# Performance work log

Measured on AMD Instinct MI355X. Metric: run time of the kernel, lower is better.

Reference implementation:

```python
import jax, jax.numpy as jnp
import numpy as np

N_NODES = 100000
N_EDGES = 1600000
N_GRAPHS = 256
IN_F = 64   # global_features (GNN input dim)
OUT_F = 64  # node_features (GNN output dim)


def setup_inputs() -> dict:
    key = jax.random.key(0)
    ks = jax.random.split(key, 8)
    x = jax.random.normal(ks[0], (N_NODES, IN_F), dtype=jnp.float32)
    edge_index = jax.random.randint(ks[1], (2, N_EDGES), 0, N_NODES, dtype=jnp.int64)
    batch = jnp.sort(jax.random.randint(ks[2], (N_NODES,), 0, N_GRAPHS, dtype=jnp.int64))
    # GNNLayer linear: in=global_features, out=node_features
    W_gnn = jax.random.normal(ks[3], (IN_F, OUT_F), dtype=jnp.float32) / np.sqrt(IN_F)
    b_gnn = jnp.zeros((OUT_F,), dtype=jnp.float32)
    # global_attention: Linear(node_features, 1)
    W_att = jax.random.normal(ks[4], (OUT_F, 1), dtype=jnp.float32) / np.sqrt(OUT_F)
    b_att = jnp.zeros((1,), dtype=jnp.float32)
    return {"x": x, "edge_index": edge_index, "batch": batch,
            "W_gnn": W_gnn, "b_gnn": b_gnn, "W_att": W_att, "b_att": b_att}


def reference(x, edge_index, batch, W_gnn, b_gnn, W_att, b_att):
    src, dst = edge_index[0], edge_index[1]
    # --- GNN message passing layer: aggregate neighbor features, transform ---
    agg = jax.ops.segment_sum(x[src], dst, num_segments=N_NODES)  # [N, IN_F]
    h = jax.nn.relu((x + agg) @ W_gnn + b_gnn)                    # [N, OUT_F]
    # --- attention scores + scatter softmax over batch segments ---
    scores = (h @ W_att + b_att)[:, 0]                            # [N]
    seg_max = jax.ops.segment_max(scores, batch, num_segments=N_GRAPHS)
    e = jnp.exp(scores - seg_max[batch])
    denom = jax.ops.segment_sum(e, batch, num_segments=N_GRAPHS)
    w = e / denom[batch]                                          # [N]
    # --- weighted scatter-add pooling ---
    out = jax.ops.segment_sum(w[:, None] * h, batch, num_segments=N_GRAPHS)
    return out  # [N_GRAPHS, OUT_F]
```

## Files before the change

### kernel.cpp

```cpp
#include <hip/hip_runtime.h>

#define N_NODES  100000
#define N_EDGES  1600000
#define N_GRAPHS 256
#define F        64

#define CHUNK    8192
#define NCHUNK   196
#define GBN      128
#define NB2      782
#define EDGE_CAP 2560

__device__ __forceinline__ unsigned short f2bf(float f) {
    unsigned int u = __float_as_uint(f);
    u += 0x7FFFu + ((u >> 16) & 1u);
    return (unsigned short)(u >> 16);
}
__global__ __launch_bounds__(256) void cast_kernel(
        const float* __restrict__ x, unsigned short* __restrict__ xh) {
    int i = blockIdx.x * 256 + threadIdx.x;
    float4 v = ((const float4*)x)[i];
    ushort4 o;
    o.x = f2bf(v.x); o.y = f2bf(v.y); o.z = f2bf(v.z); o.w = f2bf(v.w);
    ((ushort4*)xh)[i] = o;
}

__global__ __launch_bounds__(1024) void scatter_sort_kernel(
        const int* __restrict__ src, const int* __restrict__ dst,
        unsigned int* __restrict__ pairs, int* __restrict__ cstartT) {
    __shared__ int hist[NB2];
    __shared__ int cur[NB2];
    __shared__ int scan[1024];
    __shared__ unsigned int stage[CHUNK];
    int tid  = threadIdx.x;
    int c    = blockIdx.x;
    int base = c * CHUNK;
    int m    = min(CHUNK, N_EDGES - base);

    for (int b = tid; b < NB2; b += 1024) hist[b] = 0;
    __syncthreads();
    for (int e = tid; e < m; e += 1024)
        atomicAdd(&hist[dst[base + e] >> 7], 1);
    __syncthreads();
    scan[tid] = (tid < NB2) ? hist[tid] : 0;
    __syncthreads();
    #pragma unroll
    for (int o = 1; o < 1024; o <<= 1) {
        int u = (tid >= o) ? scan[tid - o] : 0;
        __syncthreads();
        scan[tid] += u;
        __syncthreads();
    }
    if (tid < NB2) {
        int excl = scan[tid] - hist[tid];
        cur[tid] = excl;
        cstartT[tid * NCHUNK + c] = base + excl;
    }
    if (tid == 0) cstartT[NB2 * NCHUNK + c] = base + m;
    __syncthreads();
    for (int e = tid; e < m; e += 1024) {
        int d = dst[base + e];
        int slot = atomicAdd(&cur[d >> 7], 1);
        stage[slot] = ((unsigned)(d & (GBN - 1)) << 17) | (unsigned)src[base + e];
    }
    __syncthreads();
    for (int e = tid; e < m; e += 1024)
        pairs[base + e] = stage[e];
}

__device__ __forceinline__ float bfl(unsigned int u) { return __uint_as_float(u << 16); }
__device__ __forceinline__ float bfh(unsigned int u) { return __uint_as_float(u & 0xFFFF0000u); }

__global__ __launch_bounds__(512) void gather_pool_kernel(
        const unsigned short* __restrict__ xh,
        const unsigned int*   __restrict__ pairs,
        const int*   __restrict__ cstartT,
        const int*   __restrict__ batch,
        const float* __restrict__ Wg,
        const float* __restrict__ bg,
        const float* __restrict__ Wa,
        const float* __restrict__ ba,
        float*       __restrict__ out_acc,
        float*       __restrict__ denom) {
    __shared__ int rstart[NCHUNK];
    __shared__ int rcnt[NCHUNK];
    __shared__ int roff[NCHUNK];
    __shared__ int sc[256];
    __shared__ int Etot_s;
    __shared__ unsigned int epairs[EDGE_CAP];
    __shared__ unsigned int esrc[EDGE_CAP];
    __shared__ int ncnt[GBN];
    __shared__ int nstart[GBN];
    __shared__ int ncur[GBN];

    int tid   = threadIdx.x;
    int wave  = tid >> 6;
    int lane  = tid & 63;
    int b     = blockIdx.x;
    int node0 = b * GBN;
    int nn    = min(GBN, N_NODES - node0);

    if (tid < NCHUNK) {
        int a = cstartT[b * NCHUNK + tid];
        int n = cstartT[(b + 1) * NCHUNK + tid];
        rstart[tid] = a;
        rcnt[tid]   = n - a;
    }
    __syncthreads();
    if (tid < 256) sc[tid] = (tid < NCHUNK) ? rcnt[tid] : 0;
    __syncthreads();
    #pragma unroll
    for (int o = 1; o < 256; o <<= 1) {
        int u = (tid < 256 && tid >= o) ? sc[tid - o] : 0;
        __syncthreads();
        if (tid < 256) sc[tid] += u;
        __syncthreads();
    }
    if (tid < NCHUNK) roff[tid] = sc[tid] - rcnt[tid];
    if (tid == 0) Etot_s = sc[NCHUNK - 1];
    __syncthreads();
    int E = Etot_s;

    for (int r = wave; r < NCHUNK; r += 8) {
        int cr = rcnt[r];
        for (int l = lane; l < cr; l += 64)
            epairs[roff[r] + l] = pairs[rstart[r] + l];
    }
    __syncthreads();

    if (tid < GBN) ncnt[tid] = 0;
    __syncthreads();
    for (int e = tid; e < E; e += 512)
        atomicAdd(&ncnt[epairs[e] >> 17], 1);
    __syncthreads();
    if (tid < 128) sc[tid] = ncnt[tid];
    __syncthreads();
    #pragma unroll
    for (int o = 1; o < 128; o <<= 1) {
        int u = (tid < 128 && tid >= o) ? sc[tid - o] : 0;
        __syncthreads();
        if (tid < 128) sc[tid] += u;
        __syncthreads();
    }
    if (tid < GBN) {
        int excl = sc[tid] - ncnt[tid];
        nstart[tid] = excl;
        ncur[tid]   = excl;
    }
    __syncthreads();
    for (int e = tid; e < E; e += 512) {
        unsigned int p = epairs[e];
        int slot = atomicAdd(&ncur[p >> 17], 1);
        esrc[slot] = p & 0x1FFFFu;
    }
    __syncthreads();

    int grp = lane >> 3;
    int cc  = lane & 7;

    float wcol[F];
    #pragma unroll
    for (int k = 0; k < F; ++k) wcol[k] = Wg[k * F + lane];
    float bgl = bg[lane];
    float wal = Wa[lane];
    float ba0 = ba[0];

    const uint4* xh4 = (const uint4*)xh;

    int r0 = wave * 16;
    if (r0 < nn) {
        int rEnd = min(r0 + 16, nn);
        int   cur_g = batch[node0 + r0];
        float accw  = 0.f;
        float denw  = 0.f;

        for (int r = r0; r < rEnd; ++r) {
            int n     = node0 + r;
            int start = nstart[r];
            int end   = start + ncnt[r];

            float a0=0.f,a1=0.f,a2=0.f,a3=0.f,a4=0.f,a5=0.f,a6=0.f,a7=0.f;
            for (int bs = start; bs < end; bs += 64) {
                int jmax = end - bs; if (jmax > 64) jmax = 64;
                int sl = (bs + lane < end) ? (int)esrc[bs + lane] : 0;
                for (int j = 0; j < jmax; j += 8) {
                    int el = j + grp;
                    int s  = __shfl(sl, el, 64);
                    if (el < jmax) {
                        uint4 v = xh4[s * 8 + cc];
                        a0 += bfl(v.x); a1 += bfh(v.x);
                        a2 += bfl(v.y); a3 += bfh(v.y);
                        a4 += bfl(v.z); a5 += bfh(v.z);
                        a6 += bfl(v.w); a7 += bfh(v.w);
                    }
                }
            }
            #pragma unroll
            for (int o = 8; o <= 32; o <<= 1) {
                a0 += __shfl_xor(a0, o, 64); a1 += __shfl_xor(a1, o, 64);
                a2 += __shfl_xor(a2, o, 64); a3 += __shfl_xor(a3, o, 64);
                a4 += __shfl_xor(a4, o, 64); a5 += __shfl_xor(a5, o, 64);
                a6 += __shfl_xor(a6, o, 64); a7 += __shfl_xor(a7, o, 64);
            }
            {
                uint4 v = xh4[n * 8 + cc];
                a0 += bfl(v.x); a1 += bfh(v.x);
                a2 += bfl(v.y); a3 += bfh(v.y);
                a4 += bfl(v.z); a5 += bfh(v.z);
                a6 += bfl(v.w); a7 += bfh(v.w);
            }

            float re[8] = {a0,a1,a2,a3,a4,a5,a6,a7};
            float q0=0.f,q1=0.f,q2=0.f,q3=0.f,q4=0.f,q5=0.f,q6=0.f,q7=0.f;
            #pragma unroll
            for (int k = 0; k < F; k += 8) {
                int ln = k >> 3;
                q0 += __int_as_float(__builtin_amdgcn_readlane(__float_as_int(re[0]), ln)) * wcol[k + 0];
                q1 += __int_as_float(__builtin_amdgcn_readlane(__float_as_int(re[1]), ln)) * wcol[k + 1];
                q2 += __int_as_float(__builtin_amdgcn_readlane(__float_as_int(re[2]), ln)) * wcol[k + 2];
                q3 += __int_as_float(__builtin_amdgcn_readlane(__float_as_int(re[3]), ln)) * wcol[k + 3];
                q4 += __int_as_float(__builtin_amdgcn_readlane(__float_as_int(re[4]), ln)) * wcol[k + 4];
                q5 += __int_as_float(__builtin_amdgcn_readlane(__float_as_int(re[5]), ln)) * wcol[k + 5];
                q6 += __int_as_float(__builtin_amdgcn_readlane(__float_as_int(re[6]), ln)) * wcol[k + 6];
                q7 += __int_as_float(__builtin_amdgcn_readlane(__float_as_int(re[7]), ln)) * wcol[k + 7];
            }
            float hv = ((q0 + q1) + (q2 + q3)) + ((q4 + q5) + (q6 + q7)) + bgl;
            hv = hv > 0.f ? hv : 0.f;

            float p = hv * wal;
            #pragma unroll
            for (int o = 32; o > 0; o >>= 1)
                p += __shfl_down(p, o, 64);
            float s = __int_as_float(__builtin_amdgcn_readlane(__float_as_int(p), 0)) + ba0;
            float e = __expf(s);

            int g = batch[n];
            if (g != cur_g) {
                atomicAdd(&out_acc[cur_g * F + lane], accw);
                if (lane == 0) atomicAdd(&denom[cur_g], denw);
                accw = 0.f; denw = 0.f; cur_g = g;
            }
            accw += e * hv;
            denw += e;
        }
        atomicAdd(&out_acc[cur_g * F + lane], accw);
        if (lane == 0) atomicAdd(&denom[cur_g], denw);
    }
}

__global__ __launch_bounds__(256) void finalize_kernel(
        float* __restrict__ out, const float* __restrict__ denom) {
    int i = blockIdx.x * 256 + threadIdx.x;
    if (i >= N_GRAPHS * F) return;
    float d = denom[i >> 6];
    out[i] = (d > 0.f) ? out[i] / d : 0.f;
}

extern "C" void kernel_launch(void* const* d_in, const int* in_sizes, int n_in,
                              void* d_out, int out_size, void* d_ws, size_t ws_size,
                              hipStream_t stream) {
    const float* x     = (const float*)d_in[0];
    const int*   ei    = (const int*)d_in[1];
    const int*   batch = (const int*)d_in[2];
    const float* Wg    = (const float*)d_in[3];
    const float* bg    = (const float*)d_in[4];
    const float* Wa    = (const float*)d_in[5];
    const float* ba    = (const float*)d_in[6];
    float* out = (float*)d_out;

    const int* src = ei;
    const int* dst = ei + N_EDGES;

    char* ws = (char*)d_ws;
    unsigned short* xh      = (unsigned short*)(ws);
    unsigned int*   pairs   = (unsigned int*)(ws + 12800000);
    int*            cstartT = (int*)(ws + 19200000);
    float*          denom   = (float*)(ws + 19814144);

    hipMemsetAsync(out,   0, (size_t)N_GRAPHS * F * sizeof(float), stream);
    hipMemsetAsync(denom, 0, N_GRAPHS * sizeof(float), stream);

    cast_kernel        <<<(N_NODES * F / 4) / 256, 256, 0, stream>>>(x, xh);
    scatter_sort_kernel<<<NCHUNK, 1024, 0, stream>>>(src, dst, pairs, cstartT);
    gather_pool_kernel <<<NB2, 512, 0, stream>>>(
        xh, pairs, cstartT, batch, Wg, bg, Wa, ba, out, denom);
    finalize_kernel    <<<(N_GRAPHS * F + 255) / 256, 256, 0, stream>>>(out, denom);
}
```

Baseline: 218.4 us.

## Split CSR compaction out of gather kernel and spread nodes across more waves

Moves the per-block edge bucketing and per-node sort into a separate compact_kernel that writes a global CSR (eidx, nbeg, nend). The gather/pool kernel then drops its shared-memory setup and assigns 25 nodes per wave across many more blocks, which should raise occupancy and parallelism in the gather phase. The cost is an extra launch plus a global write and reread of the edge index array. Per-wave atomics into out_acc also increase, since there are more waves.

```diff
diff --git a/kernel.cpp b/kernel.cpp
--- a/kernel.cpp
+++ b/kernel.cpp
@@ -68,13 +68,99 @@
         pairs[base + e] = stage[e];
 }
 
+__global__ __launch_bounds__(256) void compact_kernel(
+        const unsigned int* __restrict__ pairs,
+        const int* __restrict__ cstartT,
+        int* __restrict__ eidx,
+        int* __restrict__ nbeg,
+        int* __restrict__ nend) {
+    __shared__ int rstart[NCHUNK];
+    __shared__ int rcnt[NCHUNK];
+    __shared__ int roff[NCHUNK];
+    __shared__ int sc[256];
+    __shared__ int Etot_s;
+    __shared__ unsigned int epairs[EDGE_CAP];
+    __shared__ int ncnt[GBN];
+    __shared__ int ncur[GBN];
+
+    int tid   = threadIdx.x;
+    int wave  = tid >> 6;
+    int lane  = tid & 63;
+    int b     = blockIdx.x;
+    int node0 = b * GBN;
+    int nn    = min(GBN, N_NODES - node0);
+    int gbase = b * EDGE_CAP;
+
+    if (tid < NCHUNK) {
+        int a = cstartT[b * NCHUNK + tid];
+        int n = cstartT[(b + 1) * NCHUNK + tid];
+        rstart[tid] = a;
+        rcnt[tid]   = n - a;
+    }
+    __syncthreads();
+    sc[tid] = (tid < NCHUNK) ? rcnt[tid] : 0;
+    __syncthreads();
+    #pragma unroll
+    for (int o = 1; o < 256; o <<= 1) {
+        int u = (tid >= o) ? sc[tid - o] : 0;
+        __syncthreads();
+        sc[tid] += u;
+        __syncthreads();
+    }
+    if (tid < NCHUNK) roff[tid] = sc[tid] - rcnt[tid];
+    if (tid == 0) Etot_s = sc[NCHUNK - 1];
+    __syncthreads();
+    int E = Etot_s;
+
+    for (int r = wave; r < NCHUNK; r += 4) {
+        int cr = rcnt[r];
+        for (int l = lane; l < cr; l += 64)
+            epairs[roff[r] + l] = pairs[rstart[r] + l];
+    }
+    __syncthreads();
+
+    if (tid < GBN) ncnt[tid] = 0;
+    __syncthreads();
+    for (int e = tid; e < E; e += 256)
+        atomicAdd(&ncnt[epairs[e] >> 17], 1);
+    __syncthreads();
+    sc[tid] = (tid < GBN) ? ncnt[tid] : 0;
+    __syncthreads();
+    #pragma unroll
+    for (int o = 1; o < 128; o <<= 1) {
+        int u = (tid < 128 && tid >= o) ? sc[tid - o] : 0;
+        __syncthreads();
+        if (tid < 128) sc[tid] += u;
+        __syncthreads();
+    }
+    if (tid < GBN) {
+        int excl = sc[tid] - ncnt[tid];
+        ncur[tid] = excl;
+        if (tid < nn) {
+            nbeg[node0 + tid] = gbase + excl;
+            nend[node0 + tid] = gbase + excl + ncnt[tid];
+        }
+    }
+    __syncthreads();
+    for (int e = tid; e < E; e += 256) {
+        unsigned int p = epairs[e];
+        int slot = atomicAdd(&ncur[p >> 17], 1);
+        eidx[gbase + slot] = (int)(p & 0x1FFFFu);
+    }
+}
+
+#define NODES_PER_WAVE 25
+#define GT_NWAVES  (N_NODES / NODES_PER_WAVE)
+#define GT_BLOCKS  (GT_NWAVES / 4)
+
 __device__ __forceinline__ float bfl(unsigned int u) { return __uint_as_float(u << 16); }
 __device__ __forceinline__ float bfh(unsigned int u) { return __uint_as_float(u & 0xFFFF0000u); }
 
-__global__ __launch_bounds__(512) void gather_pool_kernel(
+__global__ __launch_bounds__(256) void gather_pool_kernel(
         const unsigned short* __restrict__ xh,
-        const unsigned int*   __restrict__ pairs,
-        const int*   __restrict__ cstartT,
+        const int*   __restrict__ nbeg,
+        const int*   __restrict__ nend,
+        const int*   __restrict__ eidx,
         const int*   __restrict__ batch,
         const float* __restrict__ Wg,
         const float* __restrict__ bg,
@@ -82,81 +168,15 @@
         const float* __restrict__ ba,
         float*       __restrict__ out_acc,
         float*       __restrict__ denom) {
-    __shared__ int rstart[NCHUNK];
-    __shared__ int rcnt[NCHUNK];
-    __shared__ int roff[NCHUNK];
-    __shared__ int sc[256];
-    __shared__ int Etot_s;
-    __shared__ unsigned int epairs[EDGE_CAP];
-    __shared__ unsigned int esrc[EDGE_CAP];
-    __shared__ int ncnt[GBN];
-    __shared__ int nstart[GBN];
-    __shared__ int ncur[GBN];
-
-    int tid   = threadIdx.x;
-    int wave  = tid >> 6;
-    int lane  = tid & 63;
-    int b     = blockIdx.x;
-    int node0 = b * GBN;
-    int nn    = min(GBN, N_NODES - node0);
-
-    if (tid < NCHUNK) {
-        int a = cstartT[b * NCHUNK + tid];
-        int n = cstartT[(b + 1) * NCHUNK + tid];
-        rstart[tid] = a;
-        rcnt[tid]   = n - a;
-    }
-    __syncthreads();
-    if (tid < 256) sc[tid] = (tid < NCHUNK) ? rcnt[tid] : 0;
-    __syncthreads();
-    #pragma unroll
-    for (int o = 1; o < 256; o <<= 1) {
-        int u = (tid < 256 && tid >= o) ? sc[tid - o] : 0;
-        __syncthreads();
-        if (tid < 256) sc[tid] += u;
-        __syncthreads();
-    }
-    if (tid < NCHUNK) roff[tid] = sc[tid] - rcnt[tid];
-    if (tid == 0) Etot_s = sc[NCHUNK - 1];
-    __syncthreads();
-    int E = Etot_s;
-
-    for (int r = wave; r < NCHUNK; r += 8) {
-        int cr = rcnt[r];
-        for (int l = lane; l < cr; l += 64)
-            epairs[roff[r] + l] = pairs[rstart[r] + l];
-    }
-    __syncthreads();
-
-    if (tid < GBN) ncnt[tid] = 0;
-    __syncthreads();
-    for (int e = tid; e < E; e += 512)
-        atomicAdd(&ncnt[epairs[e] >> 17], 1);
-    __syncthreads();
-    if (tid < 128) sc[tid] = ncnt[tid];
-    __syncthreads();
-    #pragma unroll
-    for (int o = 1; o < 128; o <<= 1) {
-        int u = (tid < 128 && tid >= o) ? sc[tid - o] : 0;
-        __syncthreads();
-        if (tid < 128) sc[tid] += u;
-        __syncthreads();
-    }
-    if (tid < GBN) {
-        int excl = sc[tid] - ncnt[tid];
-        nstart[tid] = excl;
-        ncur[tid]   = excl;
-    }
-    __syncthreads();
-    for (int e = tid; e < E; e += 512) {
-        unsigned int p = epairs[e];
-        int slot = atomicAdd(&ncur[p >> 17], 1);
-        esrc[slot] = p & 0x1FFFFu;
-    }
-    __syncthreads();
-
-    int grp = lane >> 3;
-    int cc  = lane & 7;
+    int tid  = threadIdx.x;
+    int lane = tid & 63;
+    int grp  = lane >> 3;
+    int c    = lane & 7;
+    int waveId = blockIdx.x * 4 + (tid >> 6);
+
+    int n0 = waveId * NODES_PER_WAVE;
+    if (n0 >= N_NODES) return;
+    int nEnd = n0 + NODES_PER_WAVE;
 
     float wcol[F];
     #pragma unroll
@@ -167,85 +187,80 @@
 
     const uint4* xh4 = (const uint4*)xh;
 
-    int r0 = wave * 16;
-    if (r0 < nn) {
-        int rEnd = min(r0 + 16, nn);
-        int   cur_g = batch[node0 + r0];
-        float accw  = 0.f;
-        float denw  = 0.f;
-
-        for (int r = r0; r < rEnd; ++r) {
-            int n     = node0 + r;
-            int start = nstart[r];
-            int end   = start + ncnt[r];
-
-            float a0=0.f,a1=0.f,a2=0.f,a3=0.f,a4=0.f,a5=0.f,a6=0.f,a7=0.f;
-            for (int bs = start; bs < end; bs += 64) {
-                int jmax = end - bs; if (jmax > 64) jmax = 64;
-                int sl = (bs + lane < end) ? (int)esrc[bs + lane] : 0;
-                for (int j = 0; j < jmax; j += 8) {
-                    int el = j + grp;
-                    int s  = __shfl(sl, el, 64);
-                    if (el < jmax) {
-                        uint4 v = xh4[s * 8 + cc];
-                        a0 += bfl(v.x); a1 += bfh(v.x);
-                        a2 += bfl(v.y); a3 += bfh(v.y);
-                        a4 += bfl(v.z); a5 += bfh(v.z);
-                        a6 += bfl(v.w); a7 += bfh(v.w);
-                    }
+    int   cur_g = batch[n0];
+    float accw  = 0.f;
+    float denw  = 0.f;
+
+    for (int n = n0; n < nEnd; ++n) {
+        int start = nbeg[n];
+        int end   = nend[n];
+
+        float a0=0.f,a1=0.f,a2=0.f,a3=0.f,a4=0.f,a5=0.f,a6=0.f,a7=0.f;
+        for (int base = start; base < end; base += 64) {
+            int jmax = end - base; if (jmax > 64) jmax = 64;
+            int sl = (base + lane < end) ? eidx[base + lane] : 0;
+            for (int j = 0; j < jmax; j += 8) {
+                int el = j + grp;
+                int s  = __shfl(sl, el, 64);
+                if (el < jmax) {
+                    uint4 v = xh4[s * 8 + c];
+                    a0 += bfl(v.x); a1 += bfh(v.x);
+                    a2 += bfl(v.y); a3 += bfh(v.y);
+                    a4 += bfl(v.z); a5 += bfh(v.z);
+                    a6 += bfl(v.w); a7 += bfh(v.w);
                 }
             }
-            #pragma unroll
-            for (int o = 8; o <= 32; o <<= 1) {
-                a0 += __shfl_xor(a0, o, 64); a1 += __shfl_xor(a1, o, 64);
-                a2 += __shfl_xor(a2, o, 64); a3 += __shfl_xor(a3, o, 64);
-                a4 += __shfl_xor(a4, o, 64); a5 += __shfl_xor(a5, o, 64);
-                a6 += __shfl_xor(a6, o, 64); a7 += __shfl_xor(a7, o, 64);
-            }
-            {
-                uint4 v = xh4[n * 8 + cc];
-                a0 += bfl(v.x); a1 += bfh(v.x);
-                a2 += bfl(v.y); a3 += bfh(v.y);
-                a4 += bfl(v.z); a5 += bfh(v.z);
-                a6 += bfl(v.w); a7 += bfh(v.w);
-            }
-
-            float re[8] = {a0,a1,a2,a3,a4,a5,a6,a7};
-            float q0=0.f,q1=0.f,q2=0.f,q3=0.f,q4=0.f,q5=0.f,q6=0.f,q7=0.f;
-            #pragma unroll
-            for (int k = 0; k < F; k += 8) {
-                int ln = k >> 3;
-                q0 += __int_as_float(__builtin_amdgcn_readlane(__float_as_int(re[0]), ln)) * wcol[k + 0];
-                q1 += __int_as_float(__builtin_amdgcn_readlane(__float_as_int(re[1]), ln)) * wcol[k + 1];
-                q2 += __int_as_float(__builtin_amdgcn_readlane(__float_as_int(re[2]), ln)) * wcol[k + 2];
-                q3 += __int_as_float(__builtin_amdgcn_readlane(__float_as_int(re[3]), ln)) * wcol[k + 3];
-                q4 += __int_as_float(__builtin_amdgcn_readlane(__float_as_int(re[4]), ln)) * wcol[k + 4];
-                q5 += __int_as_float(__builtin_amdgcn_readlane(__float_as_int(re[5]), ln)) * wcol[k + 5];
-                q6 += __int_as_float(__builtin_amdgcn_readlane(__float_as_int(re[6]), ln)) * wcol[k + 6];
-                q7 += __int_as_float(__builtin_amdgcn_readlane(__float_as_int(re[7]), ln)) * wcol[k + 7];
-            }
-            float hv = ((q0 + q1) + (q2 + q3)) + ((q4 + q5) + (q6 + q7)) + bgl;
-            hv = hv > 0.f ? hv : 0.f;
-
-            float p = hv * wal;
-            #pragma unroll
-            for (int o = 32; o > 0; o >>= 1)
-                p += __shfl_down(p, o, 64);
-            float s = __int_as_float(__builtin_amdgcn_readlane(__float_as_int(p), 0)) + ba0;
-            float e = __expf(s);
-
-            int g = batch[n];
-            if (g != cur_g) {
-                atomicAdd(&out_acc[cur_g * F + lane], accw);
-                if (lane == 0) atomicAdd(&denom[cur_g], denw);
-                accw = 0.f; denw = 0.f; cur_g = g;
-            }
-            accw += e * hv;
-            denw += e;
-        }
-        atomicAdd(&out_acc[cur_g * F + lane], accw);
-        if (lane == 0) atomicAdd(&denom[cur_g], denw);
-    }
+        }
+        #pragma unroll
+        for (int o = 8; o <= 32; o <<= 1) {
+            a0 += __shfl_xor(a0, o, 64); a1 += __shfl_xor(a1, o, 64);
+            a2 += __shfl_xor(a2, o, 64); a3 += __shfl_xor(a3, o, 64);
+            a4 += __shfl_xor(a4, o, 64); a5 += __shfl_xor(a5, o, 64);
+            a6 += __shfl_xor(a6, o, 64); a7 += __shfl_xor(a7, o, 64);
+        }
+        {
+            uint4 v = xh4[n * 8 + c];
+            a0 += bfl(v.x); a1 += bfh(v.x);
+            a2 += bfl(v.y); a3 += bfh(v.y);
+            a4 += bfl(v.z); a5 += bfh(v.z);
+            a6 += bfl(v.w); a7 += bfh(v.w);
+        }
+
+        float re[8] = {a0,a1,a2,a3,a4,a5,a6,a7};
+        float q0=0.f,q1=0.f,q2=0.f,q3=0.f,q4=0.f,q5=0.f,q6=0.f,q7=0.f;
+        #pragma unroll
+        for (int k = 0; k < F; k += 8) {
+            int ln = k >> 3;
+            q0 += __int_as_float(__builtin_amdgcn_readlane(__float_as_int(re[0]), ln)) * wcol[k + 0];
+            q1 += __int_as_float(__builtin_amdgcn_readlane(__float_as_int(re[1]), ln)) * wcol[k + 1];
+            q2 += __int_as_float(__builtin_amdgcn_readlane(__float_as_int(re[2]), ln)) * wcol[k + 2];
+            q3 += __int_as_float(__builtin_amdgcn_readlane(__float_as_int(re[3]), ln)) * wcol[k + 3];
+            q4 += __int_as_float(__builtin_amdgcn_readlane(__float_as_int(re[4]), ln)) * wcol[k + 4];
+            q5 += __int_as_float(__builtin_amdgcn_readlane(__float_as_int(re[5]), ln)) * wcol[k + 5];
+            q6 += __int_as_float(__builtin_amdgcn_readlane(__float_as_int(re[6]), ln)) * wcol[k + 6];
+            q7 += __int_as_float(__builtin_amdgcn_readlane(__float_as_int(re[7]), ln)) * wcol[k + 7];
+        }
+        float hv = ((q0 + q1) + (q2 + q3)) + ((q4 + q5) + (q6 + q7)) + bgl;
+        hv = hv > 0.f ? hv : 0.f;
+
+        float p = hv * wal;
+        #pragma unroll
+        for (int o = 32; o > 0; o >>= 1)
+            p += __shfl_down(p, o, 64);
+        float s = __int_as_float(__builtin_amdgcn_readlane(__float_as_int(p), 0)) + ba0;
+        float e = __expf(s);
+
+        int g = batch[n];
+        if (g != cur_g) {
+            atomicAdd(&out_acc[cur_g * F + lane], accw);
+            if (lane == 0) atomicAdd(&denom[cur_g], denw);
+            accw = 0.f; denw = 0.f; cur_g = g;
+        }
+        accw += e * hv;
+        denw += e;
+    }
+    atomicAdd(&out_acc[cur_g * F + lane], accw);
+    if (lane == 0) atomicAdd(&denom[cur_g], denw);
 }
 
 __global__ __launch_bounds__(256) void finalize_kernel(
@@ -275,14 +290,18 @@
     unsigned short* xh      = (unsigned short*)(ws);
     unsigned int*   pairs   = (unsigned int*)(ws + 12800000);
     int*            cstartT = (int*)(ws + 19200000);
-    float*          denom   = (float*)(ws + 19814144);
+    int*            eidx    = (int*)(ws + 19814144);
+    int*            nbeg    = (int*)(ws + 27821824);
+    int*            nend    = (int*)(ws + 28221824);
+    float*          denom   = (float*)(ws + 28621824);
 
     hipMemsetAsync(out,   0, (size_t)N_GRAPHS * F * sizeof(float), stream);
     hipMemsetAsync(denom, 0, N_GRAPHS * sizeof(float), stream);
 
     cast_kernel        <<<(N_NODES * F / 4) / 256, 256, 0, stream>>>(x, xh);
     scatter_sort_kernel<<<NCHUNK, 1024, 0, stream>>>(src, dst, pairs, cstartT);
-    gather_pool_kernel <<<NB2, 512, 0, stream>>>(
-        xh, pairs, cstartT, batch, Wg, bg, Wa, ba, out, denom);
+    compact_kernel     <<<NB2, 256, 0, stream>>>(pairs, cstartT, eidx, nbeg, nend);
+    gather_pool_kernel <<<GT_BLOCKS, 256, 0, stream>>>(
+        xh, nbeg, nend, eidx, batch, Wg, bg, Wa, ba, out, denom);
     finalize_kernel    <<<(N_GRAPHS * F + 255) / 256, 256, 0, stream>>>(out, denom);
 }
```

Measured after the change: 209.6 us. 1.04x faster.
